# Performance work log

Hardware: AMD Instinct MI355X
Metric: run time of the kernel (lower is better)

Reference implementation:

```python
import jax, jax.numpy as jnp
import numpy as np

B, C, H, W = 8, 256, 128, 128
WS = 8   # window size
NH = 8   # num heads
NEG = -1e9


def _rel_coords_table(ws):
    # continuous relative coords table, shape [1, 2ws-1, 2ws-1, 2]
    r = np.arange(-(ws - 1), ws, dtype=np.float32)
    t = np.stack(np.meshgrid(r, r, indexing='ij'), axis=-1)[None]
    t = t / (ws - 1) * 8.0
    t = np.sign(t) * np.log2(np.abs(t) + 1.0) / np.log2(8.0)
    return jnp.asarray(t, dtype=jnp.float32)


def _rel_pos_index(ws):
    coords = np.stack(np.meshgrid(np.arange(ws), np.arange(ws), indexing='ij'))  # [2,ws,ws]
    flat = coords.reshape(2, -1)
    rel = (flat[:, :, None] - flat[:, None, :]).transpose(1, 2, 0).astype(np.int64)  # [N,N,2]
    rel[..., 0] += ws - 1
    rel[..., 1] += ws - 1
    rel[..., 0] *= 2 * ws - 1
    return jnp.asarray(rel.sum(-1))  # [N,N]


def setup_inputs() -> dict:
    key = jax.random.key(0)
    ks = jax.random.split(key, 10)
    d8 = C // 8
    return {
        'x': jax.random.normal(ks[0], (B, C, H, W), jnp.float32),
        'y': jax.random.normal(ks[1], (B, C, H, W), jnp.float32),
        'Wq': jax.random.normal(ks[2], (d8, C), jnp.float32) * 0.02,
        'bq': jnp.zeros((d8,), jnp.float32),
        'Wk': jax.random.normal(ks[3], (d8, C), jnp.float32) * 0.02,
        'bk': jnp.zeros((d8,), jnp.float32),
        'Wv': jax.random.normal(ks[4], (C, C), jnp.float32) * 0.02,
        'bv': jnp.zeros((C,), jnp.float32),
        'gamma': jnp.full((1,), 0.5, jnp.float32),
        'qkv_w': jax.random.normal(ks[5], (3 * C, C), jnp.float32) * 0.02,
        'q_bias': jnp.zeros((C,), jnp.float32),
        'v_bias': jnp.zeros((C,), jnp.float32),
        'logit_scale': jnp.log(10.0 * jnp.ones((NH, 1, 1), jnp.float32)),
        'cpb_w1': jax.random.normal(ks[6], (512, 2), jnp.float32) * 0.02,
        'cpb_b1': jnp.zeros((512,), jnp.float32),
        'cpb_w2': jax.random.normal(ks[7], (NH, 512), jnp.float32) * 0.02,
        'proj_w': jax.random.normal(ks[8], (C, C), jnp.float32) * 0.02,
        'proj_b': jnp.zeros((C,), jnp.float32),
    }


def _criss_cross(x, y, Wq, bq, Wk, bk, Wv, bv, gamma):
    # 1x1 convs as einsum channel projections
    q = jnp.einsum('bchw,oc->bohw', x, Wq) + bq[None, :, None, None]
    k = jnp.einsum('bchw,oc->bohw', x, Wk) + bk[None, :, None, None]
    v = jnp.einsum('bchw,oc->bohw', y, Wv) + bv[None, :, None, None]
    h = x.shape[2]
    # column (H-axis) attention with -inf on diagonal; row (W-axis) attention
    diag = jnp.where(jnp.eye(h, dtype=bool), NEG, 0.0).astype(x.dtype)  # [H,H]
    eH = jnp.einsum('bchw,bcgw->bhwg', q, k) + diag[None, :, None, :]   # [B,H,W,H]
    eW = jnp.einsum('bchw,bchv->bhwv', q, k)                            # [B,H,W,W]
    att = jax.nn.softmax(jnp.concatenate([eH, eW], axis=3), axis=3)
    aH, aW = att[..., :h], att[..., h:]
    oH = jnp.einsum('bhwg,bcgw->bchw', aH, v)
    oW = jnp.einsum('bhwv,bchv->bchw', aW, v)
    return gamma[0] * (oH + oW) + x


def _window_attention(xw, qkv_w, q_bias, v_bias, logit_scale,
                      cpb_w1, cpb_b1, cpb_w2, proj_w, proj_b):
    B_, N, Cc = xw.shape
    hd = Cc // NH
    bias = jnp.concatenate([q_bias, jnp.zeros_like(v_bias), v_bias])
    qkv = (xw @ qkv_w.T + bias).reshape(B_, N, 3, NH, hd).transpose(2, 0, 3, 1, 4)
    q, k, v = qkv[0], qkv[1], qkv[2]  # [B_, NH, N, hd]
    qn = q / jnp.maximum(jnp.linalg.norm(q, axis=-1, keepdims=True), 1e-12)
    kn = k / jnp.maximum(jnp.linalg.norm(k, axis=-1, keepdims=True), 1e-12)
    scale = jnp.exp(jnp.minimum(logit_scale, jnp.log(jnp.float32(100.0))))  # [NH,1,1]
    attn = jnp.einsum('bhnd,bhmd->bhnm', qn, kn) * scale[None]
    # continuous relative position bias via inline MLP
    tbl = jax.nn.relu(_rel_coords_table(WS) @ cpb_w1.T + cpb_b1) @ cpb_w2.T  # [1,2ws-1,2ws-1,NH]
    tbl = tbl.reshape(-1, NH)
    rpb = tbl[_rel_pos_index(WS).reshape(-1)].reshape(N, N, NH).transpose(2, 0, 1)
    attn = jax.nn.softmax(attn + (16.0 * jax.nn.sigmoid(rpb))[None], axis=-1)
    out = jnp.einsum('bhnm,bhmd->bnhd', attn, v).reshape(B_, N, Cc)
    return out @ proj_w.T + proj_b


def reference(x, y, Wq, bq, Wk, bk, Wv, bv, gamma,
              qkv_w, q_bias, v_bias, logit_scale,
              cpb_w1, cpb_b1, cpb_w2, proj_w, proj_b):
    cc = _criss_cross(x, y, Wq, bq, Wk, bk, Wv, bv, gamma)   # [B,C,H,W]
    xh = cc.transpose(0, 2, 3, 1)                            # [B,H,W,C]
    win = xh.reshape(B, H // WS, WS, W // WS, WS, C)
    win = win.transpose(0, 1, 3, 2, 4, 5).reshape(-1, WS * WS, C)
    wa = _window_attention(win, qkv_w, q_bias, v_bias, logit_scale,
                           cpb_w1, cpb_b1, cpb_w2, proj_w, proj_b)
    out = wa.reshape(B, H // WS, W // WS, WS, WS, C)
    out = out.transpose(0, 1, 3, 2, 4, 5).reshape(B, H, W, C)
    return out.transpose(0, 3, 1, 2)                         # [B,C,H,W]
```

## Files before the change

kernel.cpp:

```cpp
#include <hip/hip_runtime.h>
#include <cstdio>
#include <cstddef>
#include <cstdint>

#define F_B 8
#define F_C 256
#define F_H 128
#define F_W 128
#define F_HW 16384

typedef __attribute__((ext_vector_type(8))) short short8;
typedef __attribute__((ext_vector_type(4))) short short4v;
typedef __attribute__((ext_vector_type(4))) float float4v;

__device__ __forceinline__ unsigned short f2bf(float f) {
  union {
    float f;
    uint32_t u;
  } v;
  v.f = f;
  return (unsigned short)((v.u + 0x7fffu + ((v.u >> 16) & 1u)) >> 16);
}

__device__ __forceinline__ float bf2f(unsigned short u) {
  union {
    uint32_t u;
    float f;
  } v;
  v.u = ((uint32_t)u) << 16;
  return v.f;
}

__device__ __forceinline__ void async_copy16(const unsigned short* g, unsigned short* l) {
  __builtin_amdgcn_global_load_lds((const __attribute__((address_space(1))) void*)g,
                                   (__attribute__((address_space(3))) void*)l, 16, 0, 0);
}

__global__ void build_aux2(const float* __restrict__ Wq, const float* __restrict__ Wk,
                           const float* __restrict__ bq, const float* __restrict__ bk,
                           const float* __restrict__ q_bias, const float* __restrict__ v_bias,
                           const float* __restrict__ Wv, const float* __restrict__ qkv_w,
                           const float* __restrict__ proj_w, unsigned short* __restrict__ qk_wb,
                           float* __restrict__ qk_b, float* __restrict__ qkv_b,
                           unsigned short* __restrict__ Wvb, unsigned short* __restrict__ qkv_wb,
                           unsigned short* __restrict__ proj_wb) {
  int t = blockIdx.x * 256 + threadIdx.x;
  if (t < 8192) {
    qk_wb[t] = f2bf(Wq[t]);
    qk_wb[8192 + t] = f2bf(Wk[t]);
  }
  if (t < 65536) {
    Wvb[t] = f2bf(Wv[t]);
    proj_wb[t] = f2bf(proj_w[t]);
  }
  if (t < 196608) qkv_wb[t] = f2bf(qkv_w[t]);
  if (t < 32) {
    qk_b[t] = bq[t];
    qk_b[32 + t] = bk[t];
  }
  if (t < 256) {
    qkv_b[t] = q_bias[t];
    qkv_b[256 + t] = 0.0f;
    qkv_b[512 + t] = v_bias[t];
  }
}

__device__ __forceinline__ float cpb_coord(int a) {
  float v = (float)(a - 7) * (8.0f / 7.0f);
  float lg = log2f(fabsf(v) + 1.0f) * (1.0f / 3.0f);
  return (v < 0.0f) ? -lg : lg;
}

__global__ void cpb_table(const float* __restrict__ w1, const float* __restrict__ b1,
                          const float* __restrict__ w2, float* __restrict__ tblS) {
  int e = blockIdx.x;
  int yi = e / 15, xi = e % 15;
  float ry = cpb_coord(yi), rx = cpb_coord(xi);
  __shared__ float hid[512];
  int t = threadIdx.x;
  for (int j = t; j < 512; j += 256) {
    float hv = w1[j * 2] * ry + w1[j * 2 + 1] * rx + b1[j];
    hid[j] = fmaxf(hv, 0.0f);
  }
  __syncthreads();
  if (t < 8) {
    float s = 0.0f;
    for (int j = 0; j < 512; j++) s += hid[j] * w2[t * 512 + j];
    tblS[e * 8 + t] = 16.0f / (1.0f + __expf(-s));
  }
}

__global__ void build_rpbt(const float* __restrict__ tblS, float* __restrict__ rpbt) {
  int t = blockIdx.x * 256 + threadIdx.x;
  int h = t >> 12, i = (t >> 6) & 63, j = t & 63;
  int e = ((i >> 3) - (j >> 3) + 7) * 15 + ((i & 7) - (j & 7) + 7);
  rpbt[t] = tblS[e * 8 + h];
}

__global__ void transpose_bf(const float* __restrict__ in, unsigned short* __restrict__ outb) {
  __shared__ float tile[32][33];
  int b = blockIdx.z;
  int p0 = blockIdx.x * 32;
  int c0 = blockIdx.y * 32;
  const float* src = in + (size_t)b * F_C * F_HW;
  int tx = threadIdx.x, ty = threadIdx.y;
#pragma unroll
  for (int i = 0; i < 4; i++) {
    tile[ty + i * 8][tx] = src[(size_t)(c0 + ty + i * 8) * F_HW + p0 + tx];
  }
  __syncthreads();
#pragma unroll
  for (int i = 0; i < 4; i++) {
    size_t idx = (size_t)b * F_HW * F_C + (size_t)(p0 + ty + i * 8) * F_C + c0 + tx;
    outb[idx] = f2bf(tile[tx][ty + i * 8]);
  }
}

template <int BN, int OUT>
__global__ __launch_bounds__(256) void gemm_mfma(const unsigned short* __restrict__ A,
                                                 const unsigned short* __restrict__ Wt,
                                                 const float* __restrict__ bias, void* Cmat,
                                                 int M, int N, int gx) {
  constexpr int WN = BN / 2;
  constexpr int NREP = WN / 16;
  __shared__ __align__(16) unsigned short As[128 * 32];
  __shared__ __align__(16) unsigned short Bs[BN * 32];
  int nwg = gridDim.x;
  int id = blockIdx.x;
  int cpx = nwg >> 3;
  int swz = (id & 7) * cpx + (id >> 3);
  int by = swz / gx;
  int bx = swz - by * gx;
  int m0 = by * 128;
  int n0 = bx * BN;
  int t = threadIdx.x;
  int wid = t >> 6, lane = t & 63;
  int wr = wid >> 1, wc = wid & 1;

  float4v acc[4][NREP] = {};

  for (int k0 = 0; k0 < 256; k0 += 32) {
    __syncthreads();
#pragma unroll
    for (int j = 0; j < 2; j++) {
      int r = wid * 32 + j * 16 + (lane >> 2);
      int kg = (lane & 3) ^ ((r >> 1) & 3);
      const unsigned short* gp = A + (size_t)(m0 + r) * 256 + k0 + kg * 8;
      async_copy16(gp, As + (wid * 32 + j * 16) * 32);
    }
#pragma unroll
    for (int j = 0; j < BN / 64; j++) {
      int r = wid * (BN / 4) + j * 16 + (lane >> 2);
      int kg = (lane & 3) ^ ((r >> 1) & 3);
      const unsigned short* gp = Wt + (size_t)(n0 + r) * 256 + k0 + kg * 8;
      async_copy16(gp, Bs + (wid * (BN / 4) + j * 16) * 32);
    }
    __syncthreads();
    short8 af[4];
#pragma unroll
    for (int mi = 0; mi < 4; mi++) {
      int row = wr * 64 + mi * 16 + (lane & 15);
      int kg = (lane >> 4) ^ ((row >> 1) & 3);
      af[mi] = *(const short8*)(As + row * 32 + kg * 8);
    }
    short8 bfr[NREP];
#pragma unroll
    for (int ni = 0; ni < NREP; ni++) {
      int col = wc * WN + ni * 16 + (lane & 15);
      int kg = (lane >> 4) ^ ((col >> 1) & 3);
      bfr[ni] = *(const short8*)(Bs + col * 32 + kg * 8);
    }
#pragma unroll
    for (int mi = 0; mi < 4; mi++)
#pragma unroll
      for (int ni = 0; ni < NREP; ni++)
        acc[mi][ni] =
            __builtin_amdgcn_mfma_f32_16x16x32_bf16(af[mi], bfr[ni], acc[mi][ni], 0, 0, 0);
  }
#pragma unroll
  for (int ni = 0; ni < NREP; ni++) {
    int col = n0 + wc * WN + ni * 16 + (lane & 15);
    float bn = bias[col];
#pragma unroll
    for (int mi = 0; mi < 4; mi++) {
      int row0 = m0 + wr * 64 + mi * 16 + (lane >> 4) * 4;
#pragma unroll
      for (int r = 0; r < 4; r++) {
        float v = acc[mi][ni][r] + bn;
        int row = row0 + r;
        if (OUT == 0) {
          ((float*)Cmat)[(size_t)row * N + col] = v;
        } else if (OUT == 1) {
          int bb = row >> 14, p = row & 16383;
          ((float*)Cmat)[((size_t)bb * N + col) * F_HW + p] = v;
        } else {
          ((unsigned short*)Cmat)[(size_t)row * N + col] = f2bf(v);
        }
      }
    }
  }
}

template <int MODE>
__global__ __launch_bounds__(256) void cc_logits(const float* __restrict__ qk,
                                                 unsigned short* __restrict__ e,
                                                 float* __restrict__ sums) {
  int x = blockIdx.x;
  int b = blockIdx.y;
  size_t base = (size_t)b * F_HW;
  __shared__ float kt[32][132];
  int t = threadIdx.x;
  {
    int gk = t >> 1, c0 = (t & 1) * 16;
    size_t krow = (MODE == 0) ? ((size_t)gk * F_W + x) : ((size_t)x * F_W + gk);
    const float4* src = (const float4*)(qk + (base + krow) * 64 + 32 + c0);
#pragma unroll
    for (int q4 = 0; q4 < 4; q4++) {
      float4 v = src[q4];
      kt[c0 + q4 * 4 + 0][gk] = v.x;
      kt[c0 + q4 * 4 + 1][gk] = v.y;
      kt[c0 + q4 * 4 + 2][gk] = v.z;
      kt[c0 + q4 * 4 + 3][gk] = v.w;
    }
  }
  __syncthreads();
  int i = t >> 1, g0 = (t & 1) * 64;
  size_t qrow = (MODE == 0) ? ((size_t)i * F_W + x) : ((size_t)x * F_W + i);
  const float4* qp = (const float4*)(qk + (base + qrow) * 64);
  float qreg[32];
#pragma unroll
  for (int q4 = 0; q4 < 8; q4++) {
    float4 v = qp[q4];
    qreg[q4 * 4 + 0] = v.x;
    qreg[q4 * 4 + 1] = v.y;
    qreg[q4 * 4 + 2] = v.z;
    qreg[q4 * 4 + 3] = v.w;
  }
  float acc[64];
#pragma unroll
  for (int g = 0; g < 64; g++) acc[g] = 0.0f;
  for (int c = 0; c < 32; c++) {
    float qv = qreg[c];
#pragma unroll
    for (int g = 0; g < 64; g++) acc[g] += qv * kt[c][g0 + g];
  }
  if (MODE == 0) {
    int d = i - g0;
    if (d >= 0 && d < 64) acc[d] = -1e9f;
  }
  unsigned short* ep = e + (base + qrow) * 256 + MODE * 128 + g0;
  float s = 0.0f;
#pragma unroll
  for (int g = 0; g < 64; g += 8) {
    short8 pk;
#pragma unroll
    for (int j = 0; j < 8; j++) {
      float ev = __expf(acc[g + j]);
      s += ev;
      pk[j] = (short)f2bf(ev);
    }
    *(short8*)(ep + g) = pk;
  }
  s += __shfl_xor(s, 1);
  if ((t & 1) == 0) sums[base + qrow] = s;
}

template <int MODE>
__global__ __launch_bounds__(256) void cc_pv_mfma(const unsigned short* __restrict__ eb,
                                                  const unsigned short* __restrict__ vtb,
                                                  const float* __restrict__ sumH,
                                                  const float* __restrict__ sumW,
                                                  const float* __restrict__ gamma,
                                                  const unsigned short* __restrict__ xb,
                                                  unsigned short* __restrict__ pob,
                                                  unsigned short* __restrict__ ccb) {
  int x = blockIdx.x, b = blockIdx.y;
  size_t base = (size_t)b * F_HW;
  __shared__ __align__(16) unsigned short As[128 * 128];
  __shared__ __align__(16) unsigned short Vs[256 * 64];
  int t = threadIdx.x;
  int wid = t >> 6, lane = t & 63;
  int wr = wid >> 1, wc = wid & 1;
  {
    int i = t >> 1, half = t & 1;
    size_t pix = (MODE == 0) ? ((size_t)i * F_W + x) : ((size_t)x * F_W + i);
    float rv = 1.0f / (sumH[base + pix] + sumW[base + pix]);
    const unsigned short* ep = eb + (base + pix) * 256 + MODE * 128 + half * 64;
    int g = ((i >> 3) & 7) ^ (i & 7);
#pragma unroll
    for (int s = 0; s < 8; s++) {
      short8 vin = *(const short8*)(ep + s * 8);
      short8 vo;
#pragma unroll
      for (int j = 0; j < 8; j++) vo[j] = (short)f2bf(bf2f((unsigned short)vin[j]) * rv);
      int slot = (half * 8 + s) ^ g;
      *(short8*)(As + i * 128 + slot * 8) = vo;
    }
  }
  float4v acc[4][8] = {};
#pragma unroll
  for (int kc = 0; kc < 2; kc++) {
    __syncthreads();
    {
      int ko = t >> 5, cj = t & 31;
      short8 rowv[8];
#pragma unroll
      for (int r = 0; r < 8; r++) {
        int kk = kc * 64 + ko * 8 + r;
        size_t pixk = (MODE == 0) ? ((size_t)kk * F_W + x) : ((size_t)x * F_W + kk);
        rowv[r] = *(const short8*)(vtb + (base + pixk) * 256 + cj * 8);
      }
#pragma unroll
      for (int j = 0; j < 8; j++) {
        short8 col;
#pragma unroll
        for (int r = 0; r < 8; r++) col[r] = rowv[r][j];
        int c = cj * 8 + j;
        int slot = ko ^ ((c >> 3) & 7) ^ (c & 7);
        *(short8*)(Vs + c * 64 + slot * 8) = col;
      }
    }
    __syncthreads();
#pragma unroll
    for (int ksub = 0; ksub < 2; ksub++) {
      short8 af[4];
#pragma unroll
      for (int mi = 0; mi < 4; mi++) {
        int i = wr * 64 + mi * 16 + (lane & 15);
        int slot = (kc * 8 + ksub * 4 + (lane >> 4)) ^ ((i >> 3) & 7) ^ (i & 7);
        af[mi] = *(const short8*)(As + i * 128 + slot * 8);
      }
      short8 bfv[8];
#pragma unroll
      for (int ni = 0; ni < 8; ni++) {
        int c = wc * 128 + ni * 16 + (lane & 15);
        int slot = (ksub * 4 + (lane >> 4)) ^ ((c >> 3) & 7) ^ (c & 7);
        bfv[ni] = *(const short8*)(Vs + c * 64 + slot * 8);
      }
#pragma unroll
      for (int mi = 0; mi < 4; mi++)
#pragma unroll
        for (int ni = 0; ni < 8; ni++)
          acc[mi][ni] =
              __builtin_amdgcn_mfma_f32_16x16x32_bf16(af[mi], bfv[ni], acc[mi][ni], 0, 0, 0);
    }
  }
  float gm = gamma[0];
#pragma unroll
  for (int mi = 0; mi < 4; mi++) {
#pragma unroll
    for (int ni = 0; ni < 8; ni++) {
#pragma unroll
      for (int r = 0; r < 4; r++) {
        int i = wr * 64 + mi * 16 + (lane >> 4) * 4 + r;
        int c = wc * 128 + ni * 16 + (lane & 15);
        size_t pix = (MODE == 0) ? ((size_t)i * F_W + x) : ((size_t)x * F_W + i);
        size_t idx = (base + pix) * 256 + c;
        if (MODE == 0) {
          pob[idx] = f2bf(acc[mi][ni][r]);
        } else {
          float v = gm * (bf2f(pob[idx]) + acc[mi][ni][r]) + bf2f(xb[idx]);
          ccb[idx] = f2bf(v);
        }
      }
    }
  }
}

__global__ __launch_bounds__(512, 2) void win_fused(
    const unsigned short* __restrict__ ccb, const unsigned short* __restrict__ qkv_wb,
    const float* __restrict__ qkv_b, const float* __restrict__ logit_scale,
    const float* __restrict__ rpbt, unsigned short* __restrict__ out) {
  __shared__ __align__(16) unsigned short As[64 * 256];
  __shared__ __align__(16) unsigned short Bs[8][2][512];
  __shared__ __align__(16) unsigned short QKV[3 * 64 * 256];
  int tid = threadIdx.x;
  int wid = tid >> 6, lane = tid & 63;
  int il = lane & 15, kg = lane >> 4;
  int win = blockIdx.x;
  int b = win >> 8, wy = (win >> 4) & 15, wx = win & 15;
  size_t pbase = (size_t)b * F_HW + (size_t)(wy * 8) * F_W + wx * 8;

#pragma unroll
  for (int i = 0; i < 4; i++) {
    int n = i * 16 + (tid >> 5);
    int slot = tid & 31;
    size_t srow = pbase + (size_t)(n >> 3) * F_W + (n & 7);
    async_copy16(ccb + srow * 256 + (size_t)(slot ^ (n & 7)) * 8, As + n * 256 + slot * 8);
  }
  __syncthreads();

  int r16 = lane >> 2, ks = lane & 3;
  int kgB = ks ^ ((r16 >> 1) & 3);
  unsigned short* Bw = &Bs[wid][0][0];
  for (int nc = 0; nc < 6; nc++) {
    int col0 = nc * 128;
    const unsigned short* wp = qkv_wb + (size_t)(col0 + wid * 16 + r16) * 256 + kgB * 8;
    async_copy16(wp, Bw + lane * 8);
    float4v acc[4] = {};
    int cur = 0;
    for (int k0 = 0; k0 < 256; k0 += 32) {
      short8 bfr = *(const short8*)(Bw + cur * 512 + il * 32 + (kg ^ ((il >> 1) & 3)) * 8);
      short8 af[4];
#pragma unroll
      for (int mi = 0; mi < 4; mi++) {
        int row = mi * 16 + il;
        int slot = ((k0 >> 3) + kg) ^ (row & 7);
        af[mi] = *(const short8*)(As + row * 256 + slot * 8);
      }
      if (k0 < 224) async_copy16(wp + k0 + 32, Bw + (cur ^ 1) * 512 + lane * 8);
      __builtin_amdgcn_s_setprio(1);
#pragma unroll
      for (int mi = 0; mi < 4; mi++)
        acc[mi] = __builtin_amdgcn_mfma_f32_16x16x32_bf16(bfr, af[mi], acc[mi], 0, 0, 0);
      __builtin_amdgcn_s_setprio(0);
      cur ^= 1;
    }
    int cg = col0 + wid * 16 + kg * 4;
    int sec = cg >> 8, cs = cg & 255;
    float4 bn4 = *(const float4*)(qkv_b + cg);
    float bns[4] = {bn4.x, bn4.y, bn4.z, bn4.w};
    unsigned short* qp = QKV + sec * 16384;
#pragma unroll
    for (int mi = 0; mi < 4; mi++) {
      int n = mi * 16 + il;
      short4v pk;
#pragma unroll
      for (int r = 0; r < 4; r++) pk[r] = (short)f2bf(acc[mi][r] + bns[r]);
      *(short4v*)(qp + n * 256 + (((cs >> 3) ^ (n & 7)) * 8) + (cs & 7)) = pk;
    }
  }
  __syncthreads();

  int hh = wid;
  unsigned short* Pl_w = QKV + wid * 4096;
  unsigned short* Vt_w = As + wid * 2048;

  short8 qb[4], ka[4];
#pragma unroll
  for (int ni = 0; ni < 4; ni++) {
    int i = ni * 16 + il;
    int so = ((hh * 4 + kg) ^ (i & 7)) * 8;
    short8 qv = *(const short8*)(QKV + i * 256 + so);
    short8 kv = *(const short8*)(QKV + 16384 + i * 256 + so);
    float qss = 0.0f, kss = 0.0f;
#pragma unroll
    for (int j = 0; j < 8; j++) {
      float qf = bf2f((unsigned short)qv[j]);
      float kf = bf2f((unsigned short)kv[j]);
      qss += qf * qf;
      kss += kf * kf;
    }
    qss += __shfl_xor(qss, 16);
    qss += __shfl_xor(qss, 32);
    kss += __shfl_xor(kss, 16);
    kss += __shfl_xor(kss, 32);
    float qinv = 1.0f / fmaxf(sqrtf(qss), 1e-12f);
    float kinv = 1.0f / fmaxf(sqrtf(kss), 1e-12f);
#pragma unroll
    for (int j = 0; j < 8; j++) {
      qb[ni][j] = (short)f2bf(bf2f((unsigned short)qv[j]) * qinv);
      ka[ni][j] = (short)f2bf(bf2f((unsigned short)kv[j]) * kinv);
    }
  }

  if (lane < 32) {
    int jb = lane >> 2, db = lane & 3;
    short8 rows[8];
#pragma unroll
    for (int r = 0; r < 8; r++) {
      rows[r] = *(const short8*)(QKV + 32768 + (jb * 8 + r) * 256 + (((hh * 4 + db) ^ r) * 8));
    }
#pragma unroll
    for (int c = 0; c < 8; c++) {
      int d = db * 8 + c;
      short8 col;
#pragma unroll
      for (int r = 0; r < 8; r++) col[r] = rows[r][c];
      *(short8*)(Vt_w + d * 64 + ((jb ^ (d & 7)) * 8)) = col;
    }
  }

  float4v sacc[4][4] = {};
#pragma unroll
  for (int mj = 0; mj < 4; mj++)
#pragma unroll
    for (int ni = 0; ni < 4; ni++)
      sacc[mj][ni] =
          __builtin_amdgcn_mfma_f32_16x16x32_bf16(ka[mj], qb[ni], sacc[mj][ni], 0, 0, 0);

  float scale = __expf(fminf(logit_scale[hh], 4.605170185988091f));
  __syncthreads();

#pragma unroll
  for (int ni = 0; ni < 4; ni++) {
    int i = ni * 16 + il;
    const float* rp = rpbt + ((size_t)hh * 64 + i) * 64;
    float sv[16];
    float mx = -1e30f;
#pragma unroll
    for (int mj = 0; mj < 4; mj++) {
      float4 rb = *(const float4*)(rp + mj * 16 + kg * 4);
      float rbs[4] = {rb.x, rb.y, rb.z, rb.w};
#pragma unroll
      for (int r = 0; r < 4; r++) {
        float v = sacc[mj][ni][r] * scale + rbs[r];
        sv[mj * 4 + r] = v;
        mx = fmaxf(mx, v);
      }
    }
    mx = fmaxf(mx, __shfl_xor(mx, 16));
    mx = fmaxf(mx, __shfl_xor(mx, 32));
    float sm = 0.0f;
#pragma unroll
    for (int u = 0; u < 16; u++) {
      sv[u] = __expf(sv[u] - mx);
      sm += sv[u];
    }
    sm += __shfl_xor(sm, 16);
    sm += __shfl_xor(sm, 32);
    float inv = 1.0f / sm;
#pragma unroll
    for (int mj = 0; mj < 4; mj++) {
      int j0 = mj * 16 + kg * 4;
      short4v pk;
#pragma unroll
      for (int r = 0; r < 4; r++) pk[r] = (short)f2bf(sv[mj * 4 + r] * inv);
      int byteoff = i * 128 + (((j0 >> 3) ^ (i & 7)) * 16) + (j0 & 7) * 2;
      *(short4v*)((char*)Pl_w + byteoff) = pk;
    }
  }
  __syncthreads();

  float4v oacc[2][4] = {};
#pragma unroll
  for (int kc = 0; kc < 2; kc++) {
    short8 va[2];
#pragma unroll
    for (int md = 0; md < 2; md++) {
      int d = md * 16 + il;
      va[md] = *(const short8*)((char*)Vt_w + d * 128 + (((kc * 4 + kg) ^ (d & 7)) * 16));
    }
    short8 pb[4];
#pragma unroll
    for (int ni = 0; ni < 4; ni++) {
      int i = ni * 16 + il;
      pb[ni] = *(const short8*)((char*)Pl_w + i * 128 + (((kc * 4 + kg) ^ (i & 7)) * 16));
    }
#pragma unroll
    for (int md = 0; md < 2; md++)
#pragma unroll
      for (int ni = 0; ni < 4; ni++)
        oacc[md][ni] =
            __builtin_amdgcn_mfma_f32_16x16x32_bf16(va[md], pb[ni], oacc[md][ni], 0, 0, 0);
  }

#pragma unroll
  for (int ni = 0; ni < 4; ni++) {
    int i = ni * 16 + il;
    size_t orow = (pbase + (size_t)(i >> 3) * F_W + (i & 7)) * 256 + hh * 32;
#pragma unroll
    for (int md = 0; md < 2; md++) {
      int d0 = md * 16 + kg * 4;
      short4v pk;
#pragma unroll
      for (int r = 0; r < 4; r++) pk[r] = (short)f2bf(oacc[md][ni][r]);
      *(short4v*)(out + orow + d0) = pk;
    }
  }
}

extern "C" void kernel_launch(void* const* d_in, const int* in_sizes, int n_in,
                              void* d_out, int out_size, void* d_ws, size_t ws_size,
                              hipStream_t stream) {
  const float* x = (const float*)d_in[0];
  const float* y = (const float*)d_in[1];
  const float* Wq = (const float*)d_in[2];
  const float* bq = (const float*)d_in[3];
  const float* Wk = (const float*)d_in[4];
  const float* bk = (const float*)d_in[5];
  const float* Wv = (const float*)d_in[6];
  const float* bv = (const float*)d_in[7];
  const float* gamma = (const float*)d_in[8];
  const float* qkv_w = (const float*)d_in[9];
  const float* q_bias = (const float*)d_in[10];
  const float* v_bias = (const float*)d_in[11];
  const float* logit_scale = (const float*)d_in[12];
  const float* cpb_w1 = (const float*)d_in[13];
  const float* cpb_b1 = (const float*)d_in[14];
  const float* cpb_w2 = (const float*)d_in[15];
  const float* proj_w = (const float*)d_in[16];
  const float* proj_b = (const float*)d_in[17];

  float* ws = (float*)d_ws;
  const size_t NPX = (size_t)F_B * F_HW;
  const size_t M1 = NPX * 256;
  size_t f_xb = 0;
  size_t f_ytb = M1 / 2;
  size_t f_vtb = M1;
  size_t f_pob = M1 + M1 / 2;
  size_t f_ccb = 2 * M1;
  size_t f_qkb = 2 * M1 + M1 / 2;
  size_t f_wts = f_qkb + NPX * 64;
  size_t o_qkwb = f_wts;
  size_t o_Wvb = o_qkwb + 8192;
  size_t o_qkvwb = o_Wvb + 32768;
  size_t o_projwb = o_qkvwb + 98304;
  size_t o_qkb2 = o_projwb + 32768;
  size_t o_qkvb2 = o_qkb2 + 64;
  size_t o_tbl = o_qkvb2 + 768;
  size_t o_sumH = o_tbl + 1800;
  size_t o_sumW = o_sumH + NPX;
  size_t o_rpbt = o_sumW + NPX;
  size_t need = (o_rpbt + 32768) * sizeof(float);
  if (ws_size < need) {
    fprintf(stderr, "kernel_launch: ws too small: %zu < %zu\n", ws_size, need);
    return;
  }
  unsigned short* xb = (unsigned short*)(ws + f_xb);
  unsigned short* ytb = (unsigned short*)(ws + f_ytb);
  unsigned short* eb = (unsigned short*)(ws + f_ytb);
  unsigned short* vtb = (unsigned short*)(ws + f_vtb);
  unsigned short* pob = (unsigned short*)(ws + f_pob);
  unsigned short* attn_b = (unsigned short*)(ws + f_pob);
  unsigned short* ccb = (unsigned short*)(ws + f_ccb);
  float* qkb = ws + f_qkb;
  unsigned short* qk_wb = (unsigned short*)(ws + o_qkwb);
  unsigned short* Wvb = (unsigned short*)(ws + o_Wvb);
  unsigned short* qkv_wb = (unsigned short*)(ws + o_qkvwb);
  unsigned short* proj_wb = (unsigned short*)(ws + o_projwb);
  float* qk_b = ws + o_qkb2;
  float* qkv_b = ws + o_qkvb2;
  float* tblS = ws + o_tbl;
  float* sumH = ws + o_sumH;
  float* sumW = ws + o_sumW;
  float* rpbt = ws + o_rpbt;

  build_aux2<<<dim3(768), dim3(256), 0, stream>>>(Wq, Wk, bq, bk, q_bias, v_bias, Wv, qkv_w,
                                                  proj_w, qk_wb, qk_b, qkv_b, Wvb, qkv_wb,
                                                  proj_wb);
  cpb_table<<<dim3(225), dim3(256), 0, stream>>>(cpb_w1, cpb_b1, cpb_w2, tblS);
  build_rpbt<<<dim3(128), dim3(256), 0, stream>>>(tblS, rpbt);
  transpose_bf<<<dim3(512, 8, 8), dim3(32, 8), 0, stream>>>(x, xb);
  transpose_bf<<<dim3(512, 8, 8), dim3(32, 8), 0, stream>>>(y, ytb);
  gemm_mfma<64, 0><<<dim3(1024), dim3(256), 0, stream>>>(xb, qk_wb, qk_b, qkb, (int)NPX, 64,
                                                         1);
  gemm_mfma<128, 2><<<dim3(2048), dim3(256), 0, stream>>>(ytb, Wvb, bv, vtb, (int)NPX, 256, 2);
  cc_logits<0><<<dim3(128, 8), dim3(256), 0, stream>>>(qkb, eb, sumH);
  cc_logits<1><<<dim3(128, 8), dim3(256), 0, stream>>>(qkb, eb, sumW);
  cc_pv_mfma<0><<<dim3(128, 8), dim3(256), 0, stream>>>(eb, vtb, sumH, sumW, gamma, xb, pob,
                                                        ccb);
  cc_pv_mfma<1><<<dim3(128, 8), dim3(256), 0, stream>>>(eb, vtb, sumH, sumW, gamma, xb, pob,
                                                        ccb);
  win_fused<<<dim3(2048), dim3(512), 0, stream>>>(ccb, qkv_wb, qkv_b, logit_scale, rpbt,
                                                  attn_b);
  gemm_mfma<128, 1><<<dim3(2048), dim3(256), 0, stream>>>(attn_b, proj_wb, proj_b, d_out,
                                                          (int)NPX, 256, 2);
}
```

Before: 584.2 us.

## Widen QKV GEMM per-warp tile and write V transposed directly from registers

The QKV projection in the window-attention kernel now has each warp compute 32 output columns per section instead of 16. Each A-fragment load from shared memory therefore feeds two MFMAs, and the loop runs 3 times instead of 6. The V section is no longer staged in shared memory. Each warp keeps its head's V accumulators in registers after the barrier and scatters them straight into the transposed Vt layout, which removes the old load-and-transpose pass and shrinks the QKV shared buffer. The trade-offs are more accumulator registers held live across the barrier, which could pressure the 2-blocks-per-SM launch bound, and scalar 2-byte LDS stores for the V transpose.

```diff
diff --git a/kernel.cpp b/kernel.cpp
--- a/kernel.cpp
+++ b/kernel.cpp
@@ -372,8 +372,8 @@
     const float* __restrict__ qkv_b, const float* __restrict__ logit_scale,
     const float* __restrict__ rpbt, unsigned short* __restrict__ out) {
   __shared__ __align__(16) unsigned short As[64 * 256];
-  __shared__ __align__(16) unsigned short Bs[8][2][512];
-  __shared__ __align__(16) unsigned short QKV[3 * 64 * 256];
+  __shared__ __align__(16) unsigned short Bs[8][2][1024];
+  __shared__ __align__(16) unsigned short QKV[2 * 64 * 256];
   int tid = threadIdx.x;
   int wid = tid >> 6, lane = tid & 63;
   int il = lane & 15, kg = lane >> 4;
@@ -393,14 +393,22 @@
   int r16 = lane >> 2, ks = lane & 3;
   int kgB = ks ^ ((r16 >> 1) & 3);
   unsigned short* Bw = &Bs[wid][0][0];
-  for (int nc = 0; nc < 6; nc++) {
-    int col0 = nc * 128;
-    const unsigned short* wp = qkv_wb + (size_t)(col0 + wid * 16 + r16) * 256 + kgB * 8;
+  float4v a0[4], a1[4];
+  for (int sec = 0; sec < 3; sec++) {
+    const unsigned short* wp = qkv_wb + (size_t)(sec * 256 + wid * 32 + r16) * 256 + kgB * 8;
     async_copy16(wp, Bw + lane * 8);
-    float4v acc[4] = {};
+    async_copy16(wp + 16 * 256, Bw + 512 + lane * 8);
+#pragma unroll
+    for (int mi = 0; mi < 4; mi++) {
+      float4v z = {0.0f, 0.0f, 0.0f, 0.0f};
+      a0[mi] = z;
+      a1[mi] = z;
+    }
     int cur = 0;
     for (int k0 = 0; k0 < 256; k0 += 32) {
-      short8 bfr = *(const short8*)(Bw + cur * 512 + il * 32 + (kg ^ ((il >> 1) & 3)) * 8);
+      int swB = (kg ^ ((il >> 1) & 3)) * 8;
+      short8 bf0 = *(const short8*)(Bw + cur * 1024 + il * 32 + swB);
+      short8 bf1 = *(const short8*)(Bw + cur * 1024 + 512 + il * 32 + swB);
       short8 af[4];
 #pragma unroll
       for (int mi = 0; mi < 4; mi++) {
@@ -408,26 +416,36 @@
         int slot = ((k0 >> 3) + kg) ^ (row & 7);
         af[mi] = *(const short8*)(As + row * 256 + slot * 8);
       }
-      if (k0 < 224) async_copy16(wp + k0 + 32, Bw + (cur ^ 1) * 512 + lane * 8);
+      if (k0 < 224) {
+        async_copy16(wp + k0 + 32, Bw + (cur ^ 1) * 1024 + lane * 8);
+        async_copy16(wp + 16 * 256 + k0 + 32, Bw + (cur ^ 1) * 1024 + 512 + lane * 8);
+      }
       __builtin_amdgcn_s_setprio(1);
 #pragma unroll
       for (int mi = 0; mi < 4; mi++)
-        acc[mi] = __builtin_amdgcn_mfma_f32_16x16x32_bf16(bfr, af[mi], acc[mi], 0, 0, 0);
+        a0[mi] = __builtin_amdgcn_mfma_f32_16x16x32_bf16(bf0, af[mi], a0[mi], 0, 0, 0);
+#pragma unroll
+      for (int mi = 0; mi < 4; mi++)
+        a1[mi] = __builtin_amdgcn_mfma_f32_16x16x32_bf16(bf1, af[mi], a1[mi], 0, 0, 0);
       __builtin_amdgcn_s_setprio(0);
       cur ^= 1;
     }
-    int cg = col0 + wid * 16 + kg * 4;
-    int sec = cg >> 8, cs = cg & 255;
-    float4 bn4 = *(const float4*)(qkv_b + cg);
-    float bns[4] = {bn4.x, bn4.y, bn4.z, bn4.w};
-    unsigned short* qp = QKV + sec * 16384;
-#pragma unroll
-    for (int mi = 0; mi < 4; mi++) {
-      int n = mi * 16 + il;
-      short4v pk;
-#pragma unroll
-      for (int r = 0; r < 4; r++) pk[r] = (short)f2bf(acc[mi][r] + bns[r]);
-      *(short4v*)(qp + n * 256 + (((cs >> 3) ^ (n & 7)) * 8) + (cs & 7)) = pk;
+    if (sec < 2) {
+      unsigned short* qp = QKV + sec * 16384;
+#pragma unroll
+      for (int g = 0; g < 2; g++) {
+        int cs = wid * 32 + g * 16 + kg * 4;
+        float4 bn4 = *(const float4*)(qkv_b + sec * 256 + cs);
+        float bns[4] = {bn4.x, bn4.y, bn4.z, bn4.w};
+#pragma unroll
+        for (int mi = 0; mi < 4; mi++) {
+          int n = mi * 16 + il;
+          short4v pk;
+#pragma unroll
+          for (int r = 0; r < 4; r++) pk[r] = (short)f2bf((g ? a1 : a0)[mi][r] + bns[r]);
+          *(short4v*)(qp + n * 256 + (((cs >> 3) ^ (n & 7)) * 8) + (cs & 7)) = pk;
+        }
+      }
     }
   }
   __syncthreads();
@@ -435,6 +453,23 @@
   int hh = wid;
   unsigned short* Pl_w = QKV + wid * 4096;
   unsigned short* Vt_w = As + wid * 2048;
+
+#pragma unroll
+  for (int g = 0; g < 2; g++) {
+    int cs = wid * 32 + g * 16 + kg * 4;
+    float4 bn4 = *(const float4*)(qkv_b + 512 + cs);
+    float bns[4] = {bn4.x, bn4.y, bn4.z, bn4.w};
+#pragma unroll
+    for (int mi = 0; mi < 4; mi++) {
+      int n = mi * 16 + il;
+#pragma unroll
+      for (int r = 0; r < 4; r++) {
+        int d = g * 16 + kg * 4 + r;
+        Vt_w[d * 64 + (((n >> 3) ^ (d & 7)) * 8) + (n & 7)] =
+            f2bf((g ? a1 : a0)[mi][r] + bns[r]);
+      }
+    }
+  }
 
   short8 qb[4], ka[4];
 #pragma unroll
@@ -461,23 +496,6 @@
     for (int j = 0; j < 8; j++) {
       qb[ni][j] = (short)f2bf(bf2f((unsigned short)qv[j]) * qinv);
       ka[ni][j] = (short)f2bf(bf2f((unsigned short)kv[j]) * kinv);
-    }
-  }
-
-  if (lane < 32) {
-    int jb = lane >> 2, db = lane & 3;
-    short8 rows[8];
-#pragma unroll
-    for (int r = 0; r < 8; r++) {
-      rows[r] = *(const short8*)(QKV + 32768 + (jb * 8 + r) * 256 + (((hh * 4 + db) ^ r) * 8));
-    }
-#pragma unroll
-    for (int c = 0; c < 8; c++) {
-      int d = db * 8 + c;
-      short8 col;
-#pragma unroll
-      for (int r = 0; r < 8; r++) col[r] = rows[r][c];
-      *(short8*)(Vt_w + d * 64 + ((jb ^ (d & 7)) * 8)) = col;
     }
   }
 
```

After: 563.7 us, median of 2. -3.5%, faster.
